# Kernel optimization log

Hardware: AMD Instinct MI355X
Metric: run time of the kernel (lower is better)

Reference implementation:

```python
import jax, jax.numpy as jnp
import numpy as np

N, T, F_IN = 20000, 8, 64
FILTERS, HEADS = 32, 4
E = 320000
LEAKY = 0.2  # PyG GATConv default negative_slope
HID = HEADS * FILTERS  # 128


def setup_inputs() -> dict:
    key = jax.random.key(0)
    ks = jax.random.split(key, 16)
    g = lambda k, shape, scale: jax.random.normal(k, shape, dtype=jnp.float32) * scale
    return {
        "x": g(ks[0], (N, T, F_IN), 1.0),
        "edge_index": jax.random.randint(ks[1], (2, E), 0, N, dtype=jnp.int32),
        # GATConv 1: lin weight, attention vectors (per head), bias
        "W1": g(ks[2], (HID, F_IN), (2.0 / F_IN) ** 0.5),
        "att_src1": g(ks[3], (HEADS, FILTERS), 0.1),
        "att_dst1": g(ks[4], (HEADS, FILTERS), 0.1),
        "b1": jnp.zeros((HID,), jnp.float32),
        # GATConv 2
        "W2": g(ks[5], (HID, HID), (2.0 / HID) ** 0.5),
        "att_src2": g(ks[6], (HEADS, FILTERS), 0.1),
        "att_dst2": g(ks[7], (HEADS, FILTERS), 0.1),
        "b2": jnp.zeros((HID,), jnp.float32),
        # MLP head
        "lw1": g(ks[8], (FILTERS, HID), (2.0 / HID) ** 0.5),
        "lb1": jnp.zeros((FILTERS,), jnp.float32),
        "lw2": g(ks[9], (1, FILTERS), (2.0 / FILTERS) ** 0.5),
        "lb2": jnp.zeros((1,), jnp.float32),
    }


def gat_layer(x, src, dst, W, a_src, a_dst, b):
    """PyG GATConv (concat=True, add_self_loops already applied to src/dst)."""
    h = (x @ W.T).reshape(N, HEADS, FILTERS)          # [N,H,F]
    es = (h * a_src).sum(-1)                          # [N,H] per-node src score
    ed = (h * a_dst).sum(-1)                          # [N,H] per-node dst score
    e = jax.nn.leaky_relu(es[src] + ed[dst], LEAKY)   # [E',H]
    # segment softmax over incoming edges per destination node
    m = jax.ops.segment_max(e, dst, num_segments=N)
    ex = jnp.exp(e - m[dst])
    denom = jax.ops.segment_sum(ex, dst, num_segments=N)
    alpha = ex / (denom[dst] + 1e-16)                 # [E',H]
    out = jax.ops.segment_sum(h[src] * alpha[:, :, None], dst, num_segments=N)
    return out.reshape(N, HID) + b


def reference(x, edge_index, W1, att_src1, att_dst1, b1,
              W2, att_src2, att_dst2, b2, lw1, lb1, lw2, lb2):
    # add self loops (PyG GATConv default add_self_loops=True)
    loop = jnp.arange(N, dtype=edge_index.dtype)
    src = jnp.concatenate([edge_index[0], loop])
    dst = jnp.concatenate([edge_index[1], loop])

    def step(_, x_t):
        h = jax.nn.elu(gat_layer(x_t, src, dst, W1, att_src1, att_dst1, b1))
        # dropout is identity in eval mode
        h = jax.nn.elu(gat_layer(h, src, dst, W2, att_src2, att_dst2, b2))
        h = jax.nn.relu(h @ lw1.T + lb1)
        y = h @ lw2.T + lb2                            # [N,1]
        return None, y

    _, ys = jax.lax.scan(step, None, jnp.transpose(x, (1, 0, 2)))  # scan over T
    return ys  # [T, N, 1] (stacked version of the original list of outputs)
```

## Files before the change

kernel.cpp:

```cpp
#include <hip/hip_runtime.h>

constexpr int cN     = 20000;
constexpr int cT     = 8;
constexpr int cFIN   = 64;
constexpr int cHEADS = 4;
constexpr int cF     = 32;
constexpr int cHID   = 128;
constexpr int cE     = 320000;
constexpr int cET    = cE + cN;
constexpr int cR     = cN * cT;
constexpr int cSCAT  = (cET + 255) / 256;
constexpr float cLEAKY = 0.2f;
constexpr float cL2E = 1.44269504088896340736f;


typedef __attribute__((ext_vector_type(8))) short bf16x8;
typedef __attribute__((ext_vector_type(4))) float f32x4;
typedef __attribute__((ext_vector_type(2))) float f32x2;

static __device__ __forceinline__ unsigned short f2bfu(float f) {
    unsigned int u;
    __builtin_memcpy(&u, &f, 4);
    u += 0x7FFFu + ((u >> 16) & 1u);
    return (unsigned short)(u >> 16);
}
static __device__ __forceinline__ f32x2 bfp2(unsigned int v) {
    unsigned int ul = v << 16, uh = v & 0xFFFF0000u;
    float lo, hi;
    __builtin_memcpy(&lo, &ul, 4);
    __builtin_memcpy(&hi, &uh, 4);
    return (f32x2){lo, hi};
}
static __device__ __forceinline__ unsigned int pack2(float lo, float hi) {
    unsigned int ul, uh;
    __builtin_memcpy(&ul, &lo, 4);
    __builtin_memcpy(&uh, &hi, 4);
    ul += 0x7FFFu + ((ul >> 16) & 1u);
    uh += 0x7FFFu + ((uh >> 16) & 1u);
    return (ul >> 16) | (uh & 0xFFFF0000u);
}
static __device__ __forceinline__ int featOf(int p) {
    return ((p >> 5) << 5) + ((p >> 1) & 15) + ((p & 1) << 4);
}

__global__ void cvt_deg_kernel(const float* W1, const float* W2, const float* lw1,
                               const float* b1, const float* b2, const int* ei,
                               unsigned short* W1b, unsigned short* W2bP,
                               unsigned short* lw1bP, float* b1P, float* b2P, int* deg) {
    int i = blockIdx.x * 256 + threadIdx.x;
    if (i < 8192) {
        W1b[i] = f2bfu(W1[i]);
    } else if (i < 8192 + 16384) {
        int jj = i - 8192;
        int c = jj >> 7, p = jj & 127;
        W2bP[jj] = f2bfu(W2[c * cHID + featOf(p)]);
    } else if (i < 8192 + 16384 + 4096) {
        int jj = i - 8192 - 16384;
        int c = jj >> 7, p = jj & 127;
        lw1bP[jj] = f2bfu(lw1[c * cHID + featOf(p)]);
    } else if (i < 8192 + 16384 + 4096 + 128) {
        int p = i - 8192 - 16384 - 4096;
        b1P[p] = b1[featOf(p)];
    } else if (i < 8192 + 16384 + 4096 + 256) {
        int p = i - 8192 - 16384 - 4096 - 128;
        b2P[p] = b2[featOf(p)];
    }
    if (i < cE) atomicAdd(&deg[ei[cE + i]], 1);
}

__global__ void scan_kernel(const int* deg, int* offs, int* cur) {
    __shared__ int sdeg[79 * 256];
    __shared__ int lds[256];
    int tid = threadIdx.x;
    #pragma unroll 4
    for (int k = 0; k < 79; k++) {
        int idx = k * 256 + tid;
        sdeg[idx] = (idx < cN) ? deg[idx] + 1 : 0;
    }
    __syncthreads();
    const int CH = 79;
    int base = tid * CH;
    int tot = 0;
    #pragma unroll 8
    for (int j = 0; j < CH; j++) tot += sdeg[base + j];
    lds[tid] = tot;
    __syncthreads();
    for (int off = 1; off < 256; off <<= 1) {
        int v = (tid >= off) ? lds[tid - off] : 0;
        __syncthreads();
        lds[tid] += v;
        __syncthreads();
    }
    int run = lds[tid] - tot;
    for (int j = 0; j < CH; j++) {
        int idx = base + j;
        if (idx < cN) { offs[idx] = run; cur[idx] = run; run += sdeg[idx]; }
    }
    if (tid == 255) offs[cN] = lds[255];
}

__global__ __launch_bounds__(256) void scatter_gemm1_kernel(
        const int* __restrict__ ei, int* __restrict__ cur, int* __restrict__ csr,
        const float* __restrict__ x, const unsigned short* __restrict__ W,
        const float* __restrict__ a_src, const float* __restrict__ a_dst,
        unsigned short* __restrict__ hb, float* __restrict__ es, float* __restrict__ ed) {
    int b = blockIdx.x;
    if (b < cSCAT) {
        int e = b * 256 + threadIdx.x;
        if (e >= cET) return;
        int s, d;
        if (e < cE) { s = ei[e]; d = ei[cE + e]; }
        else        { s = e - cE; d = s; }
        int pos = atomicAdd(&cur[d], 1);
        csr[pos] = s;
        return;
    }
    int gb   = b - cSCAT;
    int tid  = threadIdx.x;
    int wave = tid >> 6;
    int lane = tid & 63;
    int q    = lane >> 4;
    int mi   = lane & 15;
    int m0   = gb * 64 + wave * 16;

    int rho = m0 + mi;
    int t = rho / cN;
    int n = rho - t * cN;
    const float* xr = x + (size_t)n * (cT * cFIN) + t * cFIN;

    bf16x8 afrag[2];
    #pragma unroll
    for (int s = 0; s < 2; s++) {
        float4 v0 = *(const float4*)(xr + s * 32 + q * 8);
        float4 v1 = *(const float4*)(xr + s * 32 + q * 8 + 4);
        bf16x8 f;
        f[0] = (short)f2bfu(v0.x); f[1] = (short)f2bfu(v0.y);
        f[2] = (short)f2bfu(v0.z); f[3] = (short)f2bfu(v0.w);
        f[4] = (short)f2bfu(v1.x); f[5] = (short)f2bfu(v1.y);
        f[6] = (short)f2bfu(v1.z); f[7] = (short)f2bfu(v1.w);
        afrag[s] = f;
    }

    f32x4 acc[8];
    #pragma unroll
    for (int ct = 0; ct < 8; ct++) acc[ct] = (f32x4){0.f, 0.f, 0.f, 0.f};
    #pragma unroll
    for (int ct = 0; ct < 8; ct++) {
        int c = ct * 16 + mi;
        #pragma unroll
        for (int s = 0; s < 2; s++) {
            bf16x8 bfrag = *(const bf16x8*)(W + (size_t)c * cFIN + s * 32 + q * 8);
            acc[ct] = __builtin_amdgcn_mfma_f32_16x16x32_bf16(afrag[s], bfrag, acc[ct], 0, 0, 0);
        }
    }

    #pragma unroll
    for (int h = 0; h < 4; h++) {
        float a0 = a_src[h * 32 + mi], a1 = a_src[h * 32 + 16 + mi];
        float d0 = a_dst[h * 32 + mi], d1 = a_dst[h * 32 + 16 + mi];
        #pragma unroll
        for (int rr = 0; rr < 4; rr++) {
            float vs = acc[2 * h][rr] * a0 + acc[2 * h + 1][rr] * a1;
            float vd = acc[2 * h][rr] * d0 + acc[2 * h + 1][rr] * d1;
            vs += __shfl_xor(vs, 1); vs += __shfl_xor(vs, 2);
            vs += __shfl_xor(vs, 4); vs += __shfl_xor(vs, 8);
            vd += __shfl_xor(vd, 1); vd += __shfl_xor(vd, 2);
            vd += __shfl_xor(vd, 4); vd += __shfl_xor(vd, 8);
            if (mi == 0) {
                int rg = m0 + q * 4 + rr;
                es[rg * cHEADS + h] = vs * cL2E;
                ed[rg * cHEADS + h] = vd * cL2E;
            }
        }
    }

    #pragma unroll
    for (int rr = 0; rr < 4; rr++) {
        int rg = m0 + q * 4 + rr;
        unsigned short* hrow = hb + (size_t)rg * cHID;
        #pragma unroll
        for (int h = 0; h < 4; h++) {
            unsigned pv = pack2(acc[2 * h][rr], acc[2 * h + 1][rr]);
            *(unsigned*)(hrow + h * 32 + mi * 2) = pv;
        }
    }
}

static __device__ __forceinline__ void agg_core(
        const unsigned short* __restrict__ hb, const float* __restrict__ es,
        const float* __restrict__ ed, const int* __restrict__ offs,
        const int* __restrict__ csr, const float* __restrict__ bias,
        int t, int n, int j, float* r) {
    int head = j >> 2;
    int rho  = t * cN + n;
    int s0 = offs[n], s1 = offs[n + 1];
    float edn = ed[(size_t)rho * cHEADS + head];
    const char* hpc = (const char*)(hb + (size_t)t * cN * cHID);
    const char* epc = (const char*)(es + (size_t)t * cN * cHEADS);
    const char* cc  = (const char*)csr;
    unsigned jo = (unsigned)j * 16u;
    unsigned ho = (unsigned)head * 4u;

    f32x2 acc[4];
    #pragma unroll
    for (int k = 0; k < 4; k++) acc[k] = (f32x2){0.f, 0.f};
    float den = 0.f;
    int i = s0;
    for (; i + 3 < s1; i += 4) {
        unsigned io = (unsigned)i * 4u;
        int sa = *(const int*)(cc + io);
        int sb = *(const int*)(cc + io + 4u);
        int sc = *(const int*)(cc + io + 8u);
        int sd = *(const int*)(cc + io + 12u);
        uint4 ra = *(const uint4*)(hpc + (((unsigned)sa) << 8) + jo);
        uint4 rb = *(const uint4*)(hpc + (((unsigned)sb) << 8) + jo);
        uint4 rc = *(const uint4*)(hpc + (((unsigned)sc) << 8) + jo);
        uint4 rd = *(const uint4*)(hpc + (((unsigned)sd) << 8) + jo);
        float ea = *(const float*)(epc + (((unsigned)sa) << 4) + ho) + edn;
        float eb = *(const float*)(epc + (((unsigned)sb) << 4) + ho) + edn;
        float ec = *(const float*)(epc + (((unsigned)sc) << 4) + ho) + edn;
        float ee = *(const float*)(epc + (((unsigned)sd) << 4) + ho) + edn;
        ea = (ea >= 0.f) ? ea : cLEAKY * ea;
        eb = (eb >= 0.f) ? eb : cLEAKY * eb;
        ec = (ec >= 0.f) ? ec : cLEAKY * ec;
        ee = (ee >= 0.f) ? ee : cLEAKY * ee;
        float wa = __builtin_amdgcn_exp2f(ea), wb = __builtin_amdgcn_exp2f(eb);
        float wc = __builtin_amdgcn_exp2f(ec), wd = __builtin_amdgcn_exp2f(ee);
        den += wa; den += wb; den += wc; den += wd;
        f32x2 wa2 = (f32x2){wa, wa}, wb2 = (f32x2){wb, wb};
        f32x2 wc2 = (f32x2){wc, wc}, wd2 = (f32x2){wd, wd};
        acc[0] += wa2 * bfp2(ra.x); acc[1] += wa2 * bfp2(ra.y);
        acc[2] += wa2 * bfp2(ra.z); acc[3] += wa2 * bfp2(ra.w);
        acc[0] += wb2 * bfp2(rb.x); acc[1] += wb2 * bfp2(rb.y);
        acc[2] += wb2 * bfp2(rb.z); acc[3] += wb2 * bfp2(rb.w);
        acc[0] += wc2 * bfp2(rc.x); acc[1] += wc2 * bfp2(rc.y);
        acc[2] += wc2 * bfp2(rc.z); acc[3] += wc2 * bfp2(rc.w);
        acc[0] += wd2 * bfp2(rd.x); acc[1] += wd2 * bfp2(rd.y);
        acc[2] += wd2 * bfp2(rd.z); acc[3] += wd2 * bfp2(rd.w);
    }
    for (; i < s1; i++) {
        int sa = *(const int*)(cc + (unsigned)i * 4u);
        uint4 ra = *(const uint4*)(hpc + (((unsigned)sa) << 8) + jo);
        float ea = *(const float*)(epc + (((unsigned)sa) << 4) + ho) + edn;
        ea = (ea >= 0.f) ? ea : cLEAKY * ea;
        float wa = __builtin_amdgcn_exp2f(ea);
        den += wa;
        f32x2 wa2 = (f32x2){wa, wa};
        acc[0] += wa2 * bfp2(ra.x); acc[1] += wa2 * bfp2(ra.y);
        acc[2] += wa2 * bfp2(ra.z); acc[3] += wa2 * bfp2(ra.w);
    }
    float inv = 1.f / (den + 1e-16f);
    float4 b0 = *(const float4*)(bias + 8 * j);
    float4 b1v = *(const float4*)(bias + 8 * j + 4);
    float v0 = acc[0].x * inv + b0.x;  r[0] = (v0 > 0.f) ? v0 : expm1f(v0);
    float v1 = acc[0].y * inv + b0.y;  r[1] = (v1 > 0.f) ? v1 : expm1f(v1);
    float v2 = acc[1].x * inv + b0.z;  r[2] = (v2 > 0.f) ? v2 : expm1f(v2);
    float v3 = acc[1].y * inv + b0.w;  r[3] = (v3 > 0.f) ? v3 : expm1f(v3);
    float v4 = acc[2].x * inv + b1v.x; r[4] = (v4 > 0.f) ? v4 : expm1f(v4);
    float v5 = acc[2].y * inv + b1v.y; r[5] = (v5 > 0.f) ? v5 : expm1f(v5);
    float v6 = acc[3].x * inv + b1v.z; r[6] = (v6 > 0.f) ? v6 : expm1f(v6);
    float v7 = acc[3].y * inv + b1v.w; r[7] = (v7 > 0.f) ? v7 : expm1f(v7);
}

__global__ __launch_bounds__(256) void agg_gemm_kernel(
        const unsigned short* __restrict__ hb, const float* __restrict__ es,
        const float* __restrict__ ed, const int* __restrict__ offs,
        const int* __restrict__ csr, const float* __restrict__ b1P,
        const unsigned short* __restrict__ W2bP, const float* __restrict__ a_src,
        const float* __restrict__ a_dst, unsigned short* __restrict__ hb2,
        float* __restrict__ es2, float* __restrict__ ed2) {
    __shared__ unsigned short tile[16 * 128];
    int b    = blockIdx.x;
    int t    = b & 7;
    int g    = b >> 3;
    int tid  = threadIdx.x;
    int lrow = tid >> 4;
    int j    = tid & 15;
    int n0   = g * 16;

    float r[8];
    agg_core(hb, es, ed, offs, csr, b1P, t, n0 + lrow, j, r);
    {
        uint4 o;
        o.x = pack2(r[0], r[1]); o.y = pack2(r[2], r[3]);
        o.z = pack2(r[4], r[5]); o.w = pack2(r[6], r[7]);
        unsigned tb = (unsigned)lrow * 256u + (((unsigned)j * 16u) ^ (((unsigned)(lrow & 7)) << 4));
        *(uint4*)((char*)tile + tb) = o;
    }
    __syncthreads();

    int wave = tid >> 6;
    int lane = tid & 63;
    int q    = lane >> 4;
    int mi   = lane & 15;
    bf16x8 afrag[4];
    #pragma unroll
    for (int s = 0; s < 4; s++) {
        unsigned addr = (unsigned)mi * 256u +
                        (((unsigned)(s * 64 + q * 16)) ^ (((unsigned)(mi & 7)) << 4));
        afrag[s] = *(const bf16x8*)((const char*)tile + addr);
    }
    f32x4 acc2[2];
    acc2[0] = (f32x4){0.f, 0.f, 0.f, 0.f};
    acc2[1] = acc2[0];
    #pragma unroll
    for (int ct = 0; ct < 2; ct++) {
        int c = (wave * 2 + ct) * 16 + mi;
        #pragma unroll
        for (int s = 0; s < 4; s++) {
            bf16x8 bfrag = *(const bf16x8*)(W2bP + (size_t)c * cHID + s * 32 + q * 8);
            acc2[ct] = __builtin_amdgcn_mfma_f32_16x16x32_bf16(afrag[s], bfrag, acc2[ct], 0, 0, 0);
        }
    }

    {
        float a0 = a_src[wave * 32 + mi], a1 = a_src[wave * 32 + 16 + mi];
        float d0 = a_dst[wave * 32 + mi], d1 = a_dst[wave * 32 + 16 + mi];
        #pragma unroll
        for (int rr = 0; rr < 4; rr++) {
            float vs = acc2[0][rr] * a0 + acc2[1][rr] * a1;
            float vd = acc2[0][rr] * d0 + acc2[1][rr] * d1;
            vs += __shfl_xor(vs, 1); vs += __shfl_xor(vs, 2);
            vs += __shfl_xor(vs, 4); vs += __shfl_xor(vs, 8);
            vd += __shfl_xor(vd, 1); vd += __shfl_xor(vd, 2);
            vd += __shfl_xor(vd, 4); vd += __shfl_xor(vd, 8);
            if (mi == 0) {
                int rg = t * cN + n0 + q * 4 + rr;
                es2[(size_t)rg * cHEADS + wave] = vs * cL2E;
                ed2[(size_t)rg * cHEADS + wave] = vd * cL2E;
            }
        }
    }

    #pragma unroll
    for (int rr = 0; rr < 4; rr++) {
        int rg = t * cN + n0 + q * 4 + rr;
        unsigned pv = pack2(acc2[0][rr], acc2[1][rr]);
        *(unsigned*)(hb2 + (size_t)rg * cHID + wave * 32 + mi * 2) = pv;
    }
}

__global__ __launch_bounds__(256) void TemporalGAT_20005957665499_kernel(
        const unsigned short* __restrict__ hb2, const float* __restrict__ es,
        const float* __restrict__ ed, const int* __restrict__ offs,
        const int* __restrict__ csr, const float* __restrict__ b2P,
        const unsigned short* __restrict__ lw1bP, const float* __restrict__ lb1,
        const float* __restrict__ lw2, const float* __restrict__ lb2,
        float* __restrict__ out) {
    __shared__ unsigned short tile[16 * 128];
    int b    = blockIdx.x;
    int t    = b & 7;
    int g    = b >> 3;
    int tid  = threadIdx.x;
    int lrow = tid >> 4;
    int j    = tid & 15;
    int n0   = g * 16;

    float r[8];
    agg_core(hb2, es, ed, offs, csr, b2P, t, n0 + lrow, j, r);
    {
        uint4 o;
        o.x = pack2(r[0], r[1]); o.y = pack2(r[2], r[3]);
        o.z = pack2(r[4], r[5]); o.w = pack2(r[6], r[7]);
        unsigned tb = (unsigned)lrow * 256u + (((unsigned)j * 16u) ^ (((unsigned)(lrow & 7)) << 4));
        *(uint4*)((char*)tile + tb) = o;
    }
    __syncthreads();

    if (tid < 64) {
        int q  = tid >> 4;
        int mi = tid & 15;
        bf16x8 afrag[4];
        #pragma unroll
        for (int s = 0; s < 4; s++) {
            unsigned addr = (unsigned)mi * 256u +
                            (((unsigned)(s * 64 + q * 16)) ^ (((unsigned)(mi & 7)) << 4));
            afrag[s] = *(const bf16x8*)((const char*)tile + addr);
        }
        f32x4 acc2[2];
        acc2[0] = (f32x4){0.f, 0.f, 0.f, 0.f};
        acc2[1] = acc2[0];
        #pragma unroll
        for (int ct = 0; ct < 2; ct++) {
            int c = ct * 16 + mi;
            #pragma unroll
            for (int s = 0; s < 4; s++) {
                bf16x8 bfrag = *(const bf16x8*)(lw1bP + (size_t)c * cHID + s * 32 + q * 8);
                acc2[ct] = __builtin_amdgcn_mfma_f32_16x16x32_bf16(afrag[s], bfrag, acc2[ct], 0, 0, 0);
            }
        }
        float lb1a = lb1[mi], lb1b_ = lb1[16 + mi];
        float lw2a = lw2[mi], lw2b_ = lw2[16 + mi];
        float l2 = lb2[0];
        #pragma unroll
        for (int rr = 0; rr < 4; rr++) {
            float va = fmaxf(acc2[0][rr] + lb1a, 0.f);
            float vb = fmaxf(acc2[1][rr] + lb1b_, 0.f);
            float v = va * lw2a + vb * lw2b_;
            v += __shfl_xor(v, 1);
            v += __shfl_xor(v, 2);
            v += __shfl_xor(v, 4);
            v += __shfl_xor(v, 8);
            if (mi == 0) out[t * cN + n0 + q * 4 + rr] = v + l2;
        }
    }
}

extern "C" void kernel_launch(void* const* d_in, const int* in_sizes, int n_in,
                              void* d_out, int out_size, void* d_ws, size_t ws_size,
                              hipStream_t stream) {
    const float* x   = (const float*)d_in[0];
    const int*   ei  = (const int*)d_in[1];
    const float* W1  = (const float*)d_in[2];
    const float* as1 = (const float*)d_in[3];
    const float* ad1 = (const float*)d_in[4];
    const float* b1  = (const float*)d_in[5];
    const float* W2  = (const float*)d_in[6];
    const float* as2 = (const float*)d_in[7];
    const float* ad2 = (const float*)d_in[8];
    const float* b2  = (const float*)d_in[9];
    const float* lw1 = (const float*)d_in[10];
    const float* lb1 = (const float*)d_in[11];
    const float* lw2 = (const float*)d_in[12];
    const float* lb2 = (const float*)d_in[13];
    float* out = (float*)d_out;
    (void)in_sizes; (void)n_in; (void)out_size; (void)ws_size;

    char* ws = (char*)d_ws;
    size_t o = 0;
    auto carveN = [&](size_t bytes) { void* p = ws + o; o += (bytes + 255) & ~(size_t)255; return p; };
    unsigned short* hb    = (unsigned short*)carveN((size_t)cR * cHID * 2);
    unsigned short* hb2   = (unsigned short*)carveN((size_t)cR * cHID * 2);
    unsigned short* W1b   = (unsigned short*)carveN((size_t)cHID * cFIN * 2);
    unsigned short* W2bP  = (unsigned short*)carveN((size_t)cHID * cHID * 2);
    unsigned short* lw1bP = (unsigned short*)carveN((size_t)cF * cHID * 2);
    float* b1P     = (float*)carveN((size_t)cHID * 4);
    float* b2P     = (float*)carveN((size_t)cHID * 4);
    float* es1_buf = (float*)carveN((size_t)cR * cHEADS * 4);
    float* ed1_buf = (float*)carveN((size_t)cR * cHEADS * 4);
    float* es2_buf = (float*)carveN((size_t)cR * cHEADS * 4);
    float* ed2_buf = (float*)carveN((size_t)cR * cHEADS * 4);
    int*   deg     = (int*)carveN((size_t)cN * 4);
    int*   offs    = (int*)carveN((size_t)(cN + 1) * 4);
    int*   cursor  = (int*)carveN((size_t)cN * 4);
    int*   csr     = (int*)carveN((size_t)cET * 4);

    hipMemsetAsync(deg, 0, (size_t)cN * 4, stream);
    cvt_deg_kernel<<<(cE + 255) / 256, 256, 0, stream>>>(
        W1, W2, lw1, b1, b2, ei, W1b, W2bP, lw1bP, b1P, b2P, deg);
    scan_kernel<<<1, 256, 0, stream>>>(deg, offs, cursor);
    scatter_gemm1_kernel<<<cSCAT + cR / 64, 256, 0, stream>>>(
        ei, cursor, csr, x, W1b, as1, ad1, hb, es1_buf, ed1_buf);
    agg_gemm_kernel<<<(cN / 16) * cT, 256, 0, stream>>>(
        hb, es1_buf, ed1_buf, offs, csr, b1P, W2bP, as2, ad2, hb2, es2_buf, ed2_buf);
    TemporalGAT_20005957665499_kernel<<<(cN / 16) * cT, 256, 0, stream>>>(
        hb2, es2_buf, ed2_buf, offs, csr, b2P, lw1bP, lb1, lw2, lb2, out);
}
```

Baseline: 384.3 us.

## Sort nodes by degree within windows and software-pipeline CSR index loads

The scan kernel now builds a permutation that groups nodes by in-degree (capped bucket) inside windows of 800 nodes, using an LDS histogram and atomics. The two aggregation kernels take each row's node from this permutation, so the 16 rows in a block have similar edge counts and threads idle less on load imbalance. The aggregation loop also prefetches the next four CSR source indices while the current gathers are in flight. In exchange, the single-block scan does extra serial work, and reads and writes are scattered through perm, which weakens locality of the output stores and of the feature gathers.

```diff
diff --git a/kernel.cpp b/kernel.cpp
--- a/kernel.cpp
+++ b/kernel.cpp
@@ -10,6 +10,8 @@
 constexpr int cET    = cE + cN;
 constexpr int cR     = cN * cT;
 constexpr int cSCAT  = (cET + 255) / 256;
+constexpr int cWIN   = 800;
+constexpr int cNW    = cN / cWIN;
 constexpr float cLEAKY = 0.2f;
 constexpr float cL2E = 1.44269504088896340736f;
 
@@ -68,15 +70,17 @@
     if (i < cE) atomicAdd(&deg[ei[cE + i]], 1);
 }
 
-__global__ void scan_kernel(const int* deg, int* offs, int* cur) {
+__global__ void scan_kernel(const int* deg, int* offs, int* cur, int* perm) {
     __shared__ int sdeg[79 * 256];
     __shared__ int lds[256];
+    __shared__ int hbin[cNW * 64];
     int tid = threadIdx.x;
     #pragma unroll 4
     for (int k = 0; k < 79; k++) {
         int idx = k * 256 + tid;
         sdeg[idx] = (idx < cN) ? deg[idx] + 1 : 0;
     }
+    for (int k = tid; k < cNW * 64; k += 256) hbin[k] = 0;
     __syncthreads();
     const int CH = 79;
     int base = tid * CH;
@@ -97,6 +101,24 @@
         if (idx < cN) { offs[idx] = run; cur[idx] = run; run += sdeg[idx]; }
     }
     if (tid == 255) offs[cN] = lds[255];
+
+    for (int k = tid; k < cN; k += 256)
+        atomicAdd(&hbin[(k / cWIN) * 64 + min(sdeg[k], 63)], 1);
+    __syncthreads();
+    if (tid < cNW) {
+        int r2 = tid * cWIN;
+        #pragma unroll 8
+        for (int bb = 0; bb < 64; bb++) {
+            int c = hbin[tid * 64 + bb];
+            hbin[tid * 64 + bb] = r2;
+            r2 += c;
+        }
+    }
+    __syncthreads();
+    for (int k = tid; k < cN; k += 256) {
+        int pos = atomicAdd(&hbin[(k / cWIN) * 64 + min(sdeg[k], 63)], 1);
+        perm[pos] = k;
+    }
 }
 
 __global__ __launch_bounds__(256) void scatter_gemm1_kernel(
@@ -206,12 +228,17 @@
     for (int k = 0; k < 4; k++) acc[k] = (f32x2){0.f, 0.f};
     float den = 0.f;
     int i = s0;
-    for (; i + 3 < s1; i += 4) {
+    int pa = 0, pb = 0, pc2 = 0, pd = 0;
+    bool have = (i + 3 < s1);
+    if (have) {
         unsigned io = (unsigned)i * 4u;
-        int sa = *(const int*)(cc + io);
-        int sb = *(const int*)(cc + io + 4u);
-        int sc = *(const int*)(cc + io + 8u);
-        int sd = *(const int*)(cc + io + 12u);
+        pa  = *(const int*)(cc + io);
+        pb  = *(const int*)(cc + io + 4u);
+        pc2 = *(const int*)(cc + io + 8u);
+        pd  = *(const int*)(cc + io + 12u);
+    }
+    while (have) {
+        int sa = pa, sb = pb, sc = pc2, sd = pd;
         uint4 ra = *(const uint4*)(hpc + (((unsigned)sa) << 8) + jo);
         uint4 rb = *(const uint4*)(hpc + (((unsigned)sb) << 8) + jo);
         uint4 rc = *(const uint4*)(hpc + (((unsigned)sc) << 8) + jo);
@@ -220,6 +247,15 @@
         float eb = *(const float*)(epc + (((unsigned)sb) << 4) + ho) + edn;
         float ec = *(const float*)(epc + (((unsigned)sc) << 4) + ho) + edn;
         float ee = *(const float*)(epc + (((unsigned)sd) << 4) + ho) + edn;
+        i += 4;
+        have = (i + 3 < s1);
+        if (have) {
+            unsigned io = (unsigned)i * 4u;
+            pa  = *(const int*)(cc + io);
+            pb  = *(const int*)(cc + io + 4u);
+            pc2 = *(const int*)(cc + io + 8u);
+            pd  = *(const int*)(cc + io + 12u);
+        }
         ea = (ea >= 0.f) ? ea : cLEAKY * ea;
         eb = (eb >= 0.f) ? eb : cLEAKY * eb;
         ec = (ec >= 0.f) ? ec : cLEAKY * ec;
@@ -265,7 +301,8 @@
 __global__ __launch_bounds__(256) void agg_gemm_kernel(
         const unsigned short* __restrict__ hb, const float* __restrict__ es,
         const float* __restrict__ ed, const int* __restrict__ offs,
-        const int* __restrict__ csr, const float* __restrict__ b1P,
+        const int* __restrict__ csr, const int* __restrict__ perm,
+        const float* __restrict__ b1P,
         const unsigned short* __restrict__ W2bP, const float* __restrict__ a_src,
         const float* __restrict__ a_dst, unsigned short* __restrict__ hb2,
         float* __restrict__ es2, float* __restrict__ ed2) {
@@ -277,9 +314,10 @@
     int lrow = tid >> 4;
     int j    = tid & 15;
     int n0   = g * 16;
+    int n    = perm[n0 + lrow];
 
     float r[8];
-    agg_core(hb, es, ed, offs, csr, b1P, t, n0 + lrow, j, r);
+    agg_core(hb, es, ed, offs, csr, b1P, t, n, j, r);
     {
         uint4 o;
         o.x = pack2(r[0], r[1]); o.y = pack2(r[2], r[3]);
@@ -325,7 +363,7 @@
             vd += __shfl_xor(vd, 1); vd += __shfl_xor(vd, 2);
             vd += __shfl_xor(vd, 4); vd += __shfl_xor(vd, 8);
             if (mi == 0) {
-                int rg = t * cN + n0 + q * 4 + rr;
+                int rg = t * cN + perm[n0 + q * 4 + rr];
                 es2[(size_t)rg * cHEADS + wave] = vs * cL2E;
                 ed2[(size_t)rg * cHEADS + wave] = vd * cL2E;
             }
@@ -334,7 +372,7 @@
 
     #pragma unroll
     for (int rr = 0; rr < 4; rr++) {
-        int rg = t * cN + n0 + q * 4 + rr;
+        int rg = t * cN + perm[n0 + q * 4 + rr];
         unsigned pv = pack2(acc2[0][rr], acc2[1][rr]);
         *(unsigned*)(hb2 + (size_t)rg * cHID + wave * 32 + mi * 2) = pv;
     }
@@ -343,7 +381,8 @@
 __global__ __launch_bounds__(256) void TemporalGAT_20005957665499_kernel(
         const unsigned short* __restrict__ hb2, const float* __restrict__ es,
         const float* __restrict__ ed, const int* __restrict__ offs,
-        const int* __restrict__ csr, const float* __restrict__ b2P,
+        const int* __restrict__ csr, const int* __restrict__ perm,
+        const float* __restrict__ b2P,
         const unsigned short* __restrict__ lw1bP, const float* __restrict__ lb1,
         const float* __restrict__ lw2, const float* __restrict__ lb2,
         float* __restrict__ out) {
@@ -355,9 +394,10 @@
     int lrow = tid >> 4;
     int j    = tid & 15;
     int n0   = g * 16;
+    int n    = perm[n0 + lrow];
 
     float r[8];
-    agg_core(hb2, es, ed, offs, csr, b2P, t, n0 + lrow, j, r);
+    agg_core(hb2, es, ed, offs, csr, b2P, t, n, j, r);
     {
         uint4 o;
         o.x = pack2(r[0], r[1]); o.y = pack2(r[2], r[3]);
@@ -401,7 +441,7 @@
             v += __shfl_xor(v, 2);
             v += __shfl_xor(v, 4);
             v += __shfl_xor(v, 8);
-            if (mi == 0) out[t * cN + n0 + q * 4 + rr] = v + l2;
+            if (mi == 0) out[t * cN + perm[n0 + q * 4 + rr]] = v + l2;
         }
     }
 }
@@ -444,15 +484,16 @@
     int*   offs    = (int*)carveN((size_t)(cN + 1) * 4);
     int*   cursor  = (int*)carveN((size_t)cN * 4);
     int*   csr     = (int*)carveN((size_t)cET * 4);
+    int*   perm    = (int*)carveN((size_t)cN * 4);
 
     hipMemsetAsync(deg, 0, (size_t)cN * 4, stream);
     cvt_deg_kernel<<<(cE + 255) / 256, 256, 0, stream>>>(
         W1, W2, lw1, b1, b2, ei, W1b, W2bP, lw1bP, b1P, b2P, deg);
-    scan_kernel<<<1, 256, 0, stream>>>(deg, offs, cursor);
+    scan_kernel<<<1, 256, 0, stream>>>(deg, offs, cursor, perm);
     scatter_gemm1_kernel<<<cSCAT + cR / 64, 256, 0, stream>>>(
         ei, cursor, csr, x, W1b, as1, ad1, hb, es1_buf, ed1_buf);
     agg_gemm_kernel<<<(cN / 16) * cT, 256, 0, stream>>>(
-        hb, es1_buf, ed1_buf, offs, csr, b1P, W2bP, as2, ad2, hb2, es2_buf, ed2_buf);
+        hb, es1_buf, ed1_buf, offs, csr, perm, b1P, W2bP, as2, ad2, hb2, es2_buf, ed2_buf);
     TemporalGAT_20005957665499_kernel<<<(cN / 16) * cT, 256, 0, stream>>>(
-        hb2, es2_buf, ed2_buf, offs, csr, b2P, lw1bP, lb1, lw2, lb2, out);
-}
+        hb2, es2_buf, ed2_buf, offs, csr, perm, b2P, lw1bP, lb1, lw2, lb2, out);
+}
```

After: 387.1 us. About the same (+0.7%).
